# Performance work log

Hardware: AMD Instinct MI355X
Metric: run time of the kernel (lower is better)

Reference implementation:

```python
import jax, jax.numpy as jnp
import numpy as np
import math

NUM_HEADS = 16
VEC_SIZE = 1024
HEAD_DIM = VEC_SIZE // NUM_HEADS


def setup_inputs() -> dict:
    key = jax.random.key(0)
    k1, k2, k3, k4, k5 = jax.random.split(key, 5)
    B, S, D = 2, 2048, VEC_SIZE
    x = jax.random.normal(k1, (B, S, D), dtype=jnp.float32)
    # Linear params, torch-style: y = x @ W.T + b
    s1 = 1.0 / math.sqrt(D)
    W_qkv = jax.random.uniform(k2, (3 * D, D), minval=-s1, maxval=s1, dtype=jnp.float32)
    b_qkv = jax.random.uniform(k3, (3 * D,), minval=-s1, maxval=s1, dtype=jnp.float32)
    W_out = jax.random.uniform(k4, (D, D), minval=-s1, maxval=s1, dtype=jnp.float32)
    b_out = jax.random.uniform(k5, (D,), minval=-s1, maxval=s1, dtype=jnp.float32)
    return {"x": x, "W_qkv": W_qkv, "b_qkv": b_qkv, "W_out": W_out, "b_out": b_out}


def reference(x, W_qkv, b_qkv, W_out, b_out):
    B, S, D = x.shape
    H, Hd = NUM_HEADS, HEAD_DIM
    qkv = x @ W_qkv.T + b_qkv                      # [B,S,3D]
    q, k, v = jnp.split(qkv, 3, axis=-1)
    # [B,S,H,Hd] -> [B,H,S,Hd]
    q = q.reshape(B, S, H, Hd).transpose(0, 2, 1, 3)
    k = k.reshape(B, S, H, Hd).transpose(0, 2, 1, 3)
    v = v.reshape(B, S, H, Hd).transpose(0, 2, 1, 3)
    weight = jnp.einsum('bhqd,bhkd->bhqk', q, k)   # [B,H,S,S]
    causal = jnp.triu(jnp.ones((S, S), dtype=bool), k=1)
    weight = jnp.where(causal, -jnp.inf, weight)
    weight = weight / jnp.sqrt(jnp.asarray(Hd, dtype=weight.dtype))
    weight = jax.nn.softmax(weight, axis=-1)
    out = jnp.einsum('bhqk,bhkd->bhqd', weight, v)  # [B,H,S,Hd]
    out = out.transpose(0, 2, 1, 3).reshape(B, S, D)
    return out @ W_out.T + b_out
```

## Files before the change

### kernel.cpp

```cpp
#include <hip/hip_runtime.h>
#include <hip/hip_bf16.h>

typedef __attribute__((ext_vector_type(8))) short short8;
typedef __attribute__((ext_vector_type(4))) short s4v;
typedef __attribute__((ext_vector_type(4))) float floatx4;

__device__ inline floatx4 mfma_bf16(short8 a, short8 b, floatx4 c) {
  return __builtin_amdgcn_mfma_f32_16x16x32_bf16(a, b, c, 0, 0, 0);
}
__device__ inline float exp2_fast(float x) { return __builtin_amdgcn_exp2f(x); }

__device__ inline short bf16s(float f) {
  __hip_bfloat16 h = __float2bfloat16(f);
  return *reinterpret_cast<short*>(&h);
}
__device__ inline float sbf16(short s) {
  return __bfloat162float(*reinterpret_cast<__hip_bfloat16*>(&s));
}

__device__ inline void gld16(__hip_bfloat16* lds, const __hip_bfloat16* g) {
  __builtin_amdgcn_global_load_lds(
      (const __attribute__((address_space(1))) void*)g,
      (__attribute__((address_space(3))) void*)lds, 16, 0, 0);
}

__global__ __launch_bounds__(256) void cvt_all(
    const float* __restrict__ x, const float* __restrict__ wqkv,
    const float* __restrict__ wout, __hip_bfloat16* __restrict__ xb,
    __hip_bfloat16* __restrict__ wqkvb, __hip_bfloat16* __restrict__ wob) {
  const int n1 = 4194304, n2 = 3145728;
  int i = (blockIdx.x * 256 + threadIdx.x) * 8;
  const float* src;
  __hip_bfloat16* dst;
  int off;
  if (i < n1) { src = x; dst = xb; off = i; }
  else if (i < n1 + n2) { src = wqkv; dst = wqkvb; off = i - n1; }
  else { src = wout; dst = wob; off = i - n1 - n2; }
  float4 a = *reinterpret_cast<const float4*>(src + off);
  float4 b = *reinterpret_cast<const float4*>(src + off + 4);
  __hip_bfloat16 t[8];
  t[0] = __float2bfloat16(a.x); t[1] = __float2bfloat16(a.y);
  t[2] = __float2bfloat16(a.z); t[3] = __float2bfloat16(a.w);
  t[4] = __float2bfloat16(b.x); t[5] = __float2bfloat16(b.y);
  t[6] = __float2bfloat16(b.z); t[7] = __float2bfloat16(b.w);
  *reinterpret_cast<short8*>(dst + off) = *reinterpret_cast<short8*>(t);
}

template<int TN, bool OUT_BF16>
__global__ __launch_bounds__(256) void gemm_bt(
    const __hip_bfloat16* __restrict__ A, const __hip_bfloat16* __restrict__ Bt,
    const float* __restrict__ bias, void* __restrict__ Cout,
    int M, int N, int K) {
  __shared__ __align__(16) __hip_bfloat16 As[128 * 64];
  __shared__ __align__(16) __hip_bfloat16 Bs[TN * 64];
  const int tid = threadIdx.x;
  const int wave = tid >> 6, lane = tid & 63, quad = lane >> 4, l15 = lane & 15;
  const int wm = (wave >> 1) * 64, wn = (wave & 1) * (TN / 2);
  const int m0 = blockIdx.y * 128, n0 = blockIdx.x * TN;
  const int NC = TN / 32;

  floatx4 acc[4][NC];
  for (int r = 0; r < 4; ++r)
    for (int c = 0; c < NC; ++c) acc[r][c] = (floatx4){0.f, 0.f, 0.f, 0.f};

  for (int k0 = 0; k0 < K; k0 += 64) {
    __syncthreads();
    for (int it = 0; it < 4; ++it) {
      int idx = it * 256 + tid;
      int row = idx >> 3, col = ((idx & 7) ^ (row & 7)) * 8;
      gld16(&As[idx * 8], A + (size_t)(m0 + row) * K + k0 + col);
    }
    for (int it = 0; it < TN * 64 / 2048; ++it) {
      int idx = it * 256 + tid;
      int row = idx >> 3, col = ((idx & 7) ^ (row & 7)) * 8;
      gld16(&Bs[idx * 8], Bt + (size_t)(n0 + row) * K + k0 + col);
    }
    __syncthreads();
    for (int ks = 0; ks < 2; ++ks) {
      short8 af[4], bf[NC];
      for (int r = 0; r < 4; ++r) {
        int row = wm + r * 16 + l15;
        af[r] = *reinterpret_cast<const short8*>(
            &As[row * 64 + (((ks * 4 + quad) ^ (l15 & 7)) * 8)]);
      }
      for (int c = 0; c < NC; ++c) {
        int row = wn + c * 16 + l15;
        bf[c] = *reinterpret_cast<const short8*>(
            &Bs[row * 64 + (((ks * 4 + quad) ^ (l15 & 7)) * 8)]);
      }
      for (int r = 0; r < 4; ++r)
        for (int c = 0; c < NC; ++c)
          acc[r][c] = mfma_bf16(af[r], bf[c], acc[r][c]);
    }
  }

  for (int c = 0; c < NC; ++c) {
    int gn = n0 + wn + c * 16 + l15;
    float bv = bias[gn];
    for (int r = 0; r < 4; ++r)
      for (int rg = 0; rg < 4; ++rg) {
        int gm = m0 + wm + r * 16 + quad * 4 + rg;
        float v = acc[r][c][rg] + bv;
        if (OUT_BF16)
          ((__hip_bfloat16*)Cout)[(size_t)gm * N + gn] = __float2bfloat16(v);
        else
          ((float*)Cout)[(size_t)gm * N + gn] = v;
      }
  }
}

__global__ __launch_bounds__(256, 3) void flash_attn(
    const __hip_bfloat16* __restrict__ qkv, __hip_bfloat16* __restrict__ out) {
  const int S = 2048, QKV = 3072;
  const int bx = blockIdx.x;
  const int g = (blockIdx.y >> 3) + 2 * blockIdx.z;
  int qt;
  if (g == 0)      qt = bx;
  else if (g == 1) qt = 31 - bx;
  else if (g == 2) qt = (bx + 8) & 31;
  else             qt = (23 - bx) & 31;
  const int h = blockIdx.y, b = blockIdx.z;
  const int q0 = qt * 64;
  __shared__ __align__(16) short Ps[2][64 * 64];
  __shared__ __align__(16) short Ks[2][64 * 64];
  __shared__ __align__(16) short Vts[2][64 * 64];
  const int tid = threadIdx.x;
  const int wave = tid >> 6, lane = tid & 63, quad = lane >> 4, l15 = lane & 15;
  const int rx = l15 & 7;
  const __hip_bfloat16* base = qkv + (size_t)b * S * QKV;
  const float c2 = 0.18033688011112042f;
  const floatx4 zero4 = {0.f, 0.f, 0.f, 0.f};
  const int j4 = (tid >> 4) * 4, d4 = (tid & 15) * 4;

  for (int it = 0; it < 2; ++it) {
    int v = tid + it * 256;
    int row = v >> 3, cb = v & 7;
    int colp = (cb ^ (row & 7)) * 8;
    gld16((__hip_bfloat16*)&Ks[0][v * 8],
          base + (size_t)row * QKV + 1024 + h * 64 + colp);
    short8 qv = *reinterpret_cast<const short8*>(
        base + (size_t)(q0 + row) * QKV + h * 64 + cb * 8);
    short qs[8];
    for (int e = 0; e < 8; ++e) qs[e] = bf16s(sbf16(qv[e]) * c2);
    *reinterpret_cast<short8*>(&Ps[1][row * 64 + colp]) = *reinterpret_cast<short8*>(qs);
  }
  s4v vr[4];
  for (int jj = 0; jj < 4; ++jj)
    vr[jj] = *reinterpret_cast<const s4v*>(
        base + (size_t)(j4 + jj) * QKV + 2048 + h * 64 + d4);
  __syncthreads();

  short8 aq[4][2];
  for (int t4 = 0; t4 < 4; ++t4)
    for (int s = 0; s < 2; ++s)
      aq[t4][s] = *reinterpret_cast<const short8*>(
          &Ps[1][(t4 * 16 + l15) * 64 + (((s * 4 + quad) ^ rx) * 8)]);

  floatx4 o_acc[4];
  for (int m = 0; m < 4; ++m) o_acc[m] = zero4;
  float lsum4[4] = {0.f, 0.f, 0.f, 0.f};
  const int krow = 16 * wave + l15;
  const int dswz = (krow & 7) ^ ((krow >> 3) & 7);

  for (int j = 0; j <= qt; ++j) {
    const int cj = j & 1, pj = cj ^ 1;

    s4v vrn[4];
    if (j < qt) {
      const size_t r1 = (size_t)(j + 1) * 64;
      for (int it = 0; it < 2; ++it) {
        int v = tid + it * 256;
        int row = v >> 3, cb = v & 7;
        int colp = (cb ^ (row & 7)) * 8;
        gld16((__hip_bfloat16*)&Ks[pj][v * 8],
              base + (r1 + row) * QKV + 1024 + h * 64 + colp);
      }
      for (int jj = 0; jj < 4; ++jj)
        vrn[jj] = *reinterpret_cast<const s4v*>(
            base + (r1 + j4 + jj) * QKV + 2048 + h * 64 + d4);
    }

    if (j > 0) {
      for (int s = 0; s < 2; ++s) {
        short8 bv = *reinterpret_cast<const short8*>(
            &Vts[pj][krow * 64 + (((4 * s + quad) ^ dswz) * 8)]);
        for (int m = 0; m < 4; ++m) {
          short8 ap = *reinterpret_cast<const short8*>(
              &Ps[pj][(m * 16 + l15) * 64 + (((4 * s + quad) ^ rx) * 8)]);
          o_acc[m] = mfma_bf16(ap, bv, o_acc[m]);
        }
      }
    }

    short8 ak0 = *reinterpret_cast<const short8*>(
        &Ks[cj][krow * 64 + ((quad ^ rx) * 8)]);
    short8 ak1 = *reinterpret_cast<const short8*>(
        &Ks[cj][krow * 64 + (((4 + quad) ^ rx) * 8)]);
    floatx4 sc[4];
    for (int t4 = 0; t4 < 4; ++t4) {
      sc[t4] = mfma_bf16(ak0, aq[t4][0], zero4);
      sc[t4] = mfma_bf16(ak1, aq[t4][1], sc[t4]);
    }
    if (j == qt) {
      int kloc = 16 * wave + quad * 4;
      for (int t4 = 0; t4 < 4; ++t4)
        for (int rg = 0; rg < 4; ++rg)
          if (kloc + rg > t4 * 16 + l15) sc[t4][rg] = -1e30f;
    }

    const int pcol = ((2 * wave + (quad >> 1)) ^ rx) * 8 + (quad & 1) * 4;
    for (int t4 = 0; t4 < 4; ++t4) {
      short pp[4];
      for (int rg = 0; rg < 4; ++rg) {
        float p = exp2_fast(sc[t4][rg]);
        lsum4[t4] += p;
        pp[rg] = bf16s(p);
      }
      *reinterpret_cast<s4v*>(&Ps[cj][(t4 * 16 + l15) * 64 + pcol]) =
          *reinterpret_cast<s4v*>(pp);
    }

    for (int e = 0; e < 4; ++e) {
      int d = d4 + e;
      int pb = (j4 >> 3) ^ (d & 7) ^ ((d >> 3) & 7);
      s4v w4 = {vr[0][e], vr[1][e], vr[2][e], vr[3][e]};
      *reinterpret_cast<s4v*>(&Vts[cj][d * 64 + pb * 8 + (j4 & 7)]) = w4;
    }
    for (int jj = 0; jj < 4; ++jj) vr[jj] = vrn[jj];

    __syncthreads();
  }

  const int pq = qt & 1;
  for (int s = 0; s < 2; ++s) {
    short8 bv = *reinterpret_cast<const short8*>(
        &Vts[pq][krow * 64 + (((4 * s + quad) ^ dswz) * 8)]);
    for (int m = 0; m < 4; ++m) {
      short8 ap = *reinterpret_cast<const short8*>(
          &Ps[pq][(m * 16 + l15) * 64 + (((4 * s + quad) ^ rx) * 8)]);
      o_acc[m] = mfma_bf16(ap, bv, o_acc[m]);
    }
  }
  for (int t4 = 0; t4 < 4; ++t4) {
    lsum4[t4] += __shfl_xor(lsum4[t4], 16);
    lsum4[t4] += __shfl_xor(lsum4[t4], 32);
  }
  float* Lf = (float*)&Ps[pq ^ 1][0];
  if (quad == 0)
    for (int t4 = 0; t4 < 4; ++t4)
      Lf[wave * 64 + t4 * 16 + l15] = lsum4[t4];
  __syncthreads();
  if (tid < 64)
    Lf[256 + tid] = 1.0f / (Lf[tid] + Lf[64 + tid] + Lf[128 + tid] + Lf[192 + tid]);
  __syncthreads();

  const int dcol = h * 64 + krow;
  for (int m = 0; m < 4; ++m)
    for (int rg = 0; rg < 4; ++rg) {
      int q = m * 16 + quad * 4 + rg;
      out[(size_t)(b * S + q0 + q) * 1024 + dcol] =
          __float2bfloat16(o_acc[m][rg] * Lf[256 + q]);
    }
}

extern "C" void kernel_launch(void* const* d_in, const int* in_sizes, int n_in,
                              void* d_out, int out_size, void* d_ws, size_t ws_size,
                              hipStream_t stream) {
  const float* x    = (const float*)d_in[0];
  const float* Wqkv = (const float*)d_in[1];
  const float* bqkv = (const float*)d_in[2];
  const float* Wout = (const float*)d_in[3];
  const float* bout = (const float*)d_in[4];
  float* out = (float*)d_out;

  const int BS = 2 * 2048;
  const int D = 1024;
  char* ws = (char*)d_ws;
  __hip_bfloat16* xb    = (__hip_bfloat16*)(ws);
  __hip_bfloat16* wqkvb = (__hip_bfloat16*)(ws + (size_t)8  * 1048576);
  __hip_bfloat16* wob   = (__hip_bfloat16*)(ws + (size_t)14 * 1048576);
  __hip_bfloat16* qkvb  = (__hip_bfloat16*)(ws + (size_t)16 * 1048576);
  __hip_bfloat16* attnb = (__hip_bfloat16*)(ws + (size_t)40 * 1048576);

  cvt_all<<<4096, 256, 0, stream>>>(x, Wqkv, Wout, xb, wqkvb, wob);

  gemm_bt<128, true><<<dim3(3072 / 128, BS / 128), 256, 0, stream>>>(
      xb, wqkvb, bqkv, qkvb, BS, 3 * D, D);

  flash_attn<<<dim3(32, 16, 2), 256, 0, stream>>>(qkvb, attnb);

  gemm_bt<64, false><<<dim3(1024 / 64, BS / 128), 256, 0, stream>>>(
      attnb, wob, bout, out, BS, D, D);
}
```

Baseline: 192.8 us.

## Load K and V fragments directly from global into registers, drop LDS staging

Removes the shared-memory buffers for K and transposed V. Each wave now loads its MFMA operand fragments directly from global memory: K is prefetched one tile ahead as 16-byte vectors, and V is gathered with strided scalar 2-byte loads. Launch bounds are raised to 4 blocks per CU to use the freed LDS. The trade is less LDS traffic and transpose work in exchange for many uncoalesced global loads, with no latency hiding for V.

```diff
diff --git a/kernel.cpp b/kernel.cpp
--- a/kernel.cpp
+++ b/kernel.cpp
@@ -109,7 +109,7 @@
   }
 }
 
-__global__ __launch_bounds__(256, 3) void flash_attn(
+__global__ __launch_bounds__(256, 4) void flash_attn(
     const __hip_bfloat16* __restrict__ qkv, __hip_bfloat16* __restrict__ out) {
   const int S = 2048, QKV = 3072;
   const int bx = blockIdx.x;
@@ -122,32 +122,31 @@
   const int h = blockIdx.y, b = blockIdx.z;
   const int q0 = qt * 64;
   __shared__ __align__(16) short Ps[2][64 * 64];
-  __shared__ __align__(16) short Ks[2][64 * 64];
-  __shared__ __align__(16) short Vts[2][64 * 64];
   const int tid = threadIdx.x;
   const int wave = tid >> 6, lane = tid & 63, quad = lane >> 4, l15 = lane & 15;
   const int rx = l15 & 7;
   const __hip_bfloat16* base = qkv + (size_t)b * S * QKV;
   const float c2 = 0.18033688011112042f;
   const floatx4 zero4 = {0.f, 0.f, 0.f, 0.f};
-  const int j4 = (tid >> 4) * 4, d4 = (tid & 15) * 4;
+  const int krow = 16 * wave + l15;
+
+  const __hip_bfloat16* kbase = base + 1024 + h * 64;
+  const __hip_bfloat16* vbase = base + 2048 + h * 64;
 
   for (int it = 0; it < 2; ++it) {
     int v = tid + it * 256;
     int row = v >> 3, cb = v & 7;
     int colp = (cb ^ (row & 7)) * 8;
-    gld16((__hip_bfloat16*)&Ks[0][v * 8],
-          base + (size_t)row * QKV + 1024 + h * 64 + colp);
     short8 qv = *reinterpret_cast<const short8*>(
         base + (size_t)(q0 + row) * QKV + h * 64 + cb * 8);
     short qs[8];
     for (int e = 0; e < 8; ++e) qs[e] = bf16s(sbf16(qv[e]) * c2);
     *reinterpret_cast<short8*>(&Ps[1][row * 64 + colp]) = *reinterpret_cast<short8*>(qs);
   }
-  s4v vr[4];
-  for (int jj = 0; jj < 4; ++jj)
-    vr[jj] = *reinterpret_cast<const s4v*>(
-        base + (size_t)(j4 + jj) * QKV + 2048 + h * 64 + d4);
+  short8 kA0 = *reinterpret_cast<const short8*>(
+      kbase + (size_t)krow * QKV + quad * 8);
+  short8 kA1 = *reinterpret_cast<const short8*>(
+      kbase + (size_t)krow * QKV + 32 + quad * 8);
   __syncthreads();
 
   short8 aq[4][2];
@@ -159,31 +158,28 @@
   floatx4 o_acc[4];
   for (int m = 0; m < 4; ++m) o_acc[m] = zero4;
   float lsum4[4] = {0.f, 0.f, 0.f, 0.f};
-  const int krow = 16 * wave + l15;
-  const int dswz = (krow & 7) ^ ((krow >> 3) & 7);
+  short8 vA0, vA1;
 
   for (int j = 0; j <= qt; ++j) {
     const int cj = j & 1, pj = cj ^ 1;
 
-    s4v vrn[4];
+    short8 kB0, kB1, vB0, vB1;
     if (j < qt) {
-      const size_t r1 = (size_t)(j + 1) * 64;
-      for (int it = 0; it < 2; ++it) {
-        int v = tid + it * 256;
-        int row = v >> 3, cb = v & 7;
-        int colp = (cb ^ (row & 7)) * 8;
-        gld16((__hip_bfloat16*)&Ks[pj][v * 8],
-              base + (r1 + row) * QKV + 1024 + h * 64 + colp);
-      }
-      for (int jj = 0; jj < 4; ++jj)
-        vrn[jj] = *reinterpret_cast<const s4v*>(
-            base + (r1 + j4 + jj) * QKV + 2048 + h * 64 + d4);
+      const __hip_bfloat16* kp = kbase + (size_t)((j + 1) * 64 + krow) * QKV;
+      kB0 = *reinterpret_cast<const short8*>(kp + quad * 8);
+      kB1 = *reinterpret_cast<const short8*>(kp + 32 + quad * 8);
+    }
+    {
+      const __hip_bfloat16* vp = vbase + (size_t)(j * 64 + quad * 8) * QKV + krow;
+      for (int i = 0; i < 8; ++i) {
+        vB0[i] = *reinterpret_cast<const short*>(vp + (size_t)i * QKV);
+        vB1[i] = *reinterpret_cast<const short*>(vp + (size_t)(32 + i) * QKV);
+      }
     }
 
     if (j > 0) {
       for (int s = 0; s < 2; ++s) {
-        short8 bv = *reinterpret_cast<const short8*>(
-            &Vts[pj][krow * 64 + (((4 * s + quad) ^ dswz) * 8)]);
+        short8 bv = s ? vA1 : vA0;
         for (int m = 0; m < 4; ++m) {
           short8 ap = *reinterpret_cast<const short8*>(
               &Ps[pj][(m * 16 + l15) * 64 + (((4 * s + quad) ^ rx) * 8)]);
@@ -192,14 +188,10 @@
       }
     }
 
-    short8 ak0 = *reinterpret_cast<const short8*>(
-        &Ks[cj][krow * 64 + ((quad ^ rx) * 8)]);
-    short8 ak1 = *reinterpret_cast<const short8*>(
-        &Ks[cj][krow * 64 + (((4 + quad) ^ rx) * 8)]);
     floatx4 sc[4];
     for (int t4 = 0; t4 < 4; ++t4) {
-      sc[t4] = mfma_bf16(ak0, aq[t4][0], zero4);
-      sc[t4] = mfma_bf16(ak1, aq[t4][1], sc[t4]);
+      sc[t4] = mfma_bf16(kA0, aq[t4][0], zero4);
+      sc[t4] = mfma_bf16(kA1, aq[t4][1], sc[t4]);
     }
     if (j == qt) {
       int kloc = 16 * wave + quad * 4;
@@ -220,21 +212,13 @@
           *reinterpret_cast<s4v*>(pp);
     }
 
-    for (int e = 0; e < 4; ++e) {
-      int d = d4 + e;
-      int pb = (j4 >> 3) ^ (d & 7) ^ ((d >> 3) & 7);
-      s4v w4 = {vr[0][e], vr[1][e], vr[2][e], vr[3][e]};
-      *reinterpret_cast<s4v*>(&Vts[cj][d * 64 + pb * 8 + (j4 & 7)]) = w4;
-    }
-    for (int jj = 0; jj < 4; ++jj) vr[jj] = vrn[jj];
-
+    kA0 = kB0; kA1 = kB1; vA0 = vB0; vA1 = vB1;
     __syncthreads();
   }
 
   const int pq = qt & 1;
   for (int s = 0; s < 2; ++s) {
-    short8 bv = *reinterpret_cast<const short8*>(
-        &Vts[pq][krow * 64 + (((4 * s + quad) ^ dswz) * 8)]);
+    short8 bv = s ? vA1 : vA0;
     for (int m = 0; m < 4; ++m) {
       short8 ap = *reinterpret_cast<const short8*>(
           &Ps[pq][(m * 16 + l15) * 64 + (((4 * s + quad) ^ rx) * 8)]);
```

Measured after the change: 182.1 us. 5.5% less time.
